# Optimization experiments

Hardware: AMD Instinct MI355X
Metric: run time of the kernel (lower is better)

The kernel has to match this reference:

```python
import jax, jax.numpy as jnp
import numpy as np
import math

NP, MNP, BS, DIM, NH, TOPK, FF = 512, 4096, 8, 256, 8, 32, 2048
HD = DIM // NH
EPS = 1e-5


def _ln(x, w, b):
    mu = jnp.mean(x, axis=-1, keepdims=True)
    var = jnp.mean((x - mu) ** 2, axis=-1, keepdims=True)
    return (x - mu) / jnp.sqrt(var + EPS) * w + b


def _lin(x, w, b):
    return x @ w.T + b


def setup_inputs() -> dict:
    key = jax.random.key(0)
    ks = jax.random.split(key, 16)
    s = 0.02
    d = {
        "tgt": jax.random.normal(ks[0], (NP, BS, DIM), jnp.float32),
        "memory": jax.random.normal(ks[1], (MNP, BS, DIM), jnp.float32),
        "query_pos": jax.random.normal(ks[2], (NP, BS, DIM), jnp.float32),
        "key_pos": jax.random.normal(ks[3], (MNP, BS, DIM), jnp.float32),
        "cw1": jax.random.normal(ks[4], (DIM, DIM), jnp.float32) * s,
        "cb1": jnp.zeros((DIM,), jnp.float32),
        "cw2": jax.random.normal(ks[5], (DIM, DIM), jnp.float32) * s,
        "cb2": jnp.zeros((DIM,), jnp.float32),
        "cw3": jax.random.normal(ks[6], (DIM, DIM), jnp.float32) * s,
        "cb3": jnp.zeros((DIM,), jnp.float32),
        "sa_in_w": jax.random.normal(ks[7], (3 * DIM, DIM), jnp.float32) * s,
        "sa_in_b": jnp.zeros((3 * DIM,), jnp.float32),
        "sa_out_w": jax.random.normal(ks[8], (DIM, DIM), jnp.float32) * s,
        "sa_out_b": jnp.zeros((DIM,), jnp.float32),
        "ln1_w": jnp.ones((DIM,), jnp.float32),
        "ln1_b": jnp.zeros((DIM,), jnp.float32),
        "ln2_w": jnp.ones((DIM,), jnp.float32),
        "ln2_b": jnp.zeros((DIM,), jnp.float32),
        "ln3_w": jnp.ones((DIM,), jnp.float32),
        "ln3_b": jnp.zeros((DIM,), jnp.float32),
        "ff1_w": jax.random.normal(ks[9], (FF, DIM), jnp.float32) * s,
        "ff1_b": jnp.zeros((FF,), jnp.float32),
        "ff2_w": jax.random.normal(ks[10], (DIM, FF), jnp.float32) * s,
        "ff2_b": jnp.zeros((DIM,), jnp.float32),
    }
    return d


def _forward(tgt, memory, query_pos, key_pos,
             cw1, cb1, cw2, cb2, cw3, cb3,
             sa_in_w, sa_in_b, sa_out_w, sa_out_b,
             ln1_w, ln1_b, ln2_w, ln2_b, ln3_w, ln3_b,
             ff1_w, ff1_b, ff2_w, ff2_b):
    npq, bs, dim = tgt.shape
    mnp = memory.shape[0]
    scale = 1.0 / math.sqrt(HD)

    # --- top-k cosine similarity neighbor selection (indices, non-diff) ---
    x = tgt.transpose(1, 0, 2)        # [bs, np, dim]
    m = memory.transpose(1, 0, 2)     # [bs, mnp, dim]
    xn = x / jnp.linalg.norm(x, axis=2, keepdims=True)
    mn = m / jnp.linalg.norm(m, axis=2, keepdims=True)
    sim = jnp.einsum('bnd,bmd->bnm', xn, mn)          # [bs, np, mnp]
    _, rns = jax.lax.top_k(sim, TOPK)                  # [bs, np, topk]

    # --- masked cross attention ---
    qc = (tgt + query_pos).transpose(1, 0, 2)          # [bs, np, dim]
    kc = (memory + key_pos).transpose(1, 0, 2)         # [bs, mnp, dim]
    vc = m
    qh = _lin(qc, cw1, cb1).reshape(bs, npq, NH, HD).transpose(0, 2, 1, 3)   # [bs,nh,np,hd]
    kh = _lin(kc, cw2, cb2).reshape(bs, mnp, NH, HD).transpose(0, 2, 1, 3)   # [bs,nh,mnp,hd]
    vh = _lin(vc, cw3, cb3).reshape(bs, mnp, NH, HD).transpose(0, 2, 1, 3)   # [bs,nh,mnp,hd]
    w = jnp.einsum('bhnd,bhmd->bhnm', qh, kh) * scale                         # [bs,nh,np,mnp]

    b_idx = jnp.arange(bs)[:, None, None]
    n_idx = jnp.arange(npq)[None, :, None]
    mask = jnp.zeros((bs, npq, mnp), w.dtype).at[b_idx, n_idx, rns].set(1.0)  # same for all heads
    mask = mask[:, None, :, :]                                                # [bs,1,np,mnp]
    w = w * mask + (-1e9) * (1.0 - mask)
    w = jax.nn.softmax(w, axis=3)
    cross = jnp.einsum('bhnm,bhmd->bhnd', w, vh).transpose(2, 0, 1, 3).reshape(npq, bs, dim)

    t = _ln(tgt + cross, ln1_w, ln1_b)

    # --- self attention (torch nn.MultiheadAttention, q=k=t+pos, v=t) ---
    wq, wk, wv = sa_in_w[:DIM], sa_in_w[DIM:2 * DIM], sa_in_w[2 * DIM:]
    bq, bk, bv = sa_in_b[:DIM], sa_in_b[DIM:2 * DIM], sa_in_b[2 * DIM:]
    qk = t + query_pos                                 # [np, bs, dim]
    q2 = _lin(qk, wq, bq).transpose(1, 0, 2).reshape(bs, npq, NH, HD).transpose(0, 2, 1, 3)
    k2 = _lin(qk, wk, bk).transpose(1, 0, 2).reshape(bs, npq, NH, HD).transpose(0, 2, 1, 3)
    v2 = _lin(t, wv, bv).transpose(1, 0, 2).reshape(bs, npq, NH, HD).transpose(0, 2, 1, 3)
    attn = jax.nn.softmax(jnp.einsum('bhnd,bhmd->bhnm', q2, k2) * scale, axis=-1)
    sa = jnp.einsum('bhnm,bhmd->bhnd', attn, v2).transpose(2, 0, 1, 3).reshape(npq, bs, dim)
    sa = _lin(sa, sa_out_w, sa_out_b)

    t = _ln(t + sa, ln2_w, ln2_b)

    # --- FFN (exact GELU, matching torch F.gelu default) ---
    ff = _lin(jax.nn.gelu(_lin(t, ff1_w, ff1_b), approximate=False), ff2_w, ff2_b)
    t = _ln(t + ff, ln3_w, ln3_b)
    return t


def reference(tgt, memory, query_pos, key_pos,
              cw1, cb1, cw2, cb2, cw3, cb3,
              sa_in_w, sa_in_b, sa_out_w, sa_out_b,
              ln1_w, ln1_b, ln2_w, ln2_b, ln3_w, ln3_b,
              ff1_w, ff1_b, ff2_w, ff2_b):
    return _forward(tgt, memory, query_pos, key_pos,
                    cw1, cb1, cw2, cb2, cw3, cb3,
                    sa_in_w, sa_in_b, sa_out_w, sa_out_b,
                    ln1_w, ln1_b, ln2_w, ln2_b, ln3_w, ln3_b,
                    ff1_w, ff1_b, ff2_w, ff2_b)
```

## Files before the change

kernel.cpp:

```cpp
#include <hip/hip_runtime.h>
#include <math.h>

typedef unsigned short u16;
typedef unsigned int u32;
typedef __bf16 bf16x8 __attribute__((ext_vector_type(8)));
typedef float f32x4 __attribute__((ext_vector_type(4)));

#define NPQ 512
#define MNP 4096
#define BSZ 8
#define DIM 256
#define NH 8
#define HD 32
#define TOPK 32
#define FFD 2048
#define SCALE 0.17677669529663687f

__device__ __forceinline__ u16 f2bf(float f){
  u32 u = __builtin_bit_cast(u32, f);
  u = (u + 0x7FFFu + ((u >> 16) & 1u)) >> 16;
  return (u16)u;
}
__device__ __forceinline__ float bf2f(u16 h){
  u32 u = ((u32)h) << 16;
  return __builtin_bit_cast(float, u);
}
__device__ __forceinline__ float wredsum(float v){
#pragma unroll
  for (int m = 32; m; m >>= 1) v += __shfl_xor(v, m, 64);
  return v;
}
__device__ __forceinline__ float gelu_exact(float x){
  return 0.5f * x * (1.0f + erff(x * 0.70710678118654752f));
}
__device__ __forceinline__ u32 keytr(u32 u){
  return u ^ (((u32)((int)u >> 31)) | 0x80000000u);
}

__global__ __launch_bounds__(256)
void cvt_all(const float* __restrict__ s0, const float* __restrict__ s1,
             const float* __restrict__ s2, const float* __restrict__ s3,
             const float* __restrict__ s4, const float* __restrict__ s5,
             const float* __restrict__ s6, u16* __restrict__ dst){
  int i = blockIdx.x*256 + threadIdx.x;
  if (i >= 1507328) return;
  const float* s; int base;
  if      (i <  65536){ s = s0; base = 0; }
  else if (i < 131072){ s = s1; base = 65536; }
  else if (i < 196608){ s = s2; base = 131072; }
  else if (i < 393216){ s = s3; base = 196608; }
  else if (i < 458752){ s = s4; base = 393216; }
  else if (i < 983040){ s = s5; base = 458752; }
  else                { s = s6; base = 983040; }
  dst[i] = f2bf(s[i - base]);
}

__global__ __launch_bounds__(256)
void prep_tgt(const float* __restrict__ tgt, const float* __restrict__ qpos,
              u16* __restrict__ xnh, u16* __restrict__ xnl, u16* __restrict__ qc,
              const float* __restrict__ cb2, const float* __restrict__ cb3,
              float* __restrict__ cbKV){
  __shared__ float sc[4];
  int r = blockIdx.x, t = threadIdx.x;
  if (r == 0){ cbKV[t] = cb2[t]; cbKV[256 + t] = cb3[t]; }
  int b = r >> 9, n = r & 511;
  long src = ((long)n*BSZ + b)*DIM + t;
  float x = tgt[src];
  float s = wredsum(x*x);
  if ((t & 63) == 0) sc[t >> 6] = s;
  __syncthreads();
  float tot = sc[0]+sc[1]+sc[2]+sc[3];
  float xn = x / sqrtf(tot);
  u16 hi = f2bf(xn);
  long dst = (long)r*DIM + t;
  xnh[dst] = hi;
  xnl[dst] = f2bf(xn - bf2f(hi));
  qc[dst]  = f2bf(x + qpos[src]);
}

__global__ __launch_bounds__(256)
void prep_mem(const float* __restrict__ mem, const float* __restrict__ kpos,
              u16* __restrict__ mnh, u16* __restrict__ mnl,
              u16* __restrict__ kc, u16* __restrict__ vc){
  __shared__ float sc[4];
  int r = blockIdx.x, t = threadIdx.x;
  int b = r >> 12, mp = r & 4095;
  long src = ((long)mp*BSZ + b)*DIM + t;
  float x = mem[src];
  float s = wredsum(x*x);
  if ((t & 63) == 0) sc[t >> 6] = s;
  __syncthreads();
  float tot = sc[0]+sc[1]+sc[2]+sc[3];
  float xn = x / sqrtf(tot);
  u16 hi = f2bf(xn);
  long dst = (long)r*DIM + t;
  mnh[dst] = hi;
  mnl[dst] = f2bf(xn - bf2f(hi));
  kc[dst]  = f2bf(x + kpos[src]);
  vc[dst]  = f2bf(x);
}

#define BST2 72
__global__ __launch_bounds__(256, 3)
void sim_gemm(const u16* __restrict__ xnh, const u16* __restrict__ xnl,
              const u16* __restrict__ mnh, const u16* __restrict__ mnl,
              float* __restrict__ sim){
  __shared__ __align__(16) u16 Bh[128*BST2];
  __shared__ __align__(16) u16 Bl[128*BST2];
  int t = threadIdx.x, lane = t & 63, wv = t >> 6;
  int ml = lane & 15, quad = lane >> 4;
  int b = blockIdx.z;
  int tM = blockIdx.y * 128 + (wv & 1) * 64;
  int tN = blockIdx.x * 128;
  int nloc = (wv >> 1) * 64;
  const u16* Ah = xnh + ((long)b*NPQ + tM + ml)*DIM;
  const u16* Al = xnl + ((long)b*NPQ + tM + ml)*DIM;
  f32x4 acc[4][4];
  f32x4 zer = {0.f,0.f,0.f,0.f};
#pragma unroll
  for (int i = 0; i < 4; i++)
#pragma unroll
    for (int j = 0; j < 4; j++) acc[i][j] = zer;

  int srow = t >> 3, scg = t & 7;
  for (int s = 0; s < 4; s++){
    int k0 = s * 64;
    if (s) __syncthreads();
#pragma unroll
    for (int p = 0; p < 4; p++){
      int r = p*32 + srow;
      long g = ((long)b*MNP + tN + r)*DIM + k0 + scg*8;
      *(uint4*)(&Bh[r*BST2 + scg*8]) = *(const uint4*)(mnh + g);
      *(uint4*)(&Bl[r*BST2 + scg*8]) = *(const uint4*)(mnl + g);
    }
    bf16x8 ca[4], ca2[4], na[4], na2[4];
#pragma unroll
    for (int i = 0; i < 4; i++){
      ca[i]  = *(const bf16x8*)(Ah + (long)i*16*DIM + k0 + quad*8);
      ca2[i] = *(const bf16x8*)(Al + (long)i*16*DIM + k0 + quad*8);
    }
    __syncthreads();
#pragma unroll
    for (int kkh = 0; kkh < 2; kkh++){
      int kk = kkh * 32;
      if (kkh == 0){
#pragma unroll
        for (int i = 0; i < 4; i++){
          na[i]  = *(const bf16x8*)(Ah + (long)i*16*DIM + k0 + 32 + quad*8);
          na2[i] = *(const bf16x8*)(Al + (long)i*16*DIM + k0 + 32 + quad*8);
        }
      }
      bf16x8 bh[4], bl[4];
#pragma unroll
      for (int j = 0; j < 4; j++){
        int nr = nloc + j*16 + ml;
        bh[j] = *(const bf16x8*)(&Bh[nr*BST2 + kk + quad*8]);
        bl[j] = *(const bf16x8*)(&Bl[nr*BST2 + kk + quad*8]);
      }
#pragma unroll
      for (int i = 0; i < 4; i++)
#pragma unroll
        for (int j = 0; j < 4; j++){
          acc[i][j] = __builtin_amdgcn_mfma_f32_16x16x32_bf16(ca[i],  bh[j], acc[i][j], 0, 0, 0);
          acc[i][j] = __builtin_amdgcn_mfma_f32_16x16x32_bf16(ca[i],  bl[j], acc[i][j], 0, 0, 0);
          acc[i][j] = __builtin_amdgcn_mfma_f32_16x16x32_bf16(ca2[i], bh[j], acc[i][j], 0, 0, 0);
        }
#pragma unroll
      for (int i = 0; i < 4; i++){ ca[i] = na[i]; ca2[i] = na2[i]; }
    }
  }
  long zC = (long)b * NPQ * MNP;
#pragma unroll
  for (int i = 0; i < 4; i++)
#pragma unroll
    for (int r = 0; r < 4; r++){
      int row = tM + i*16 + quad*4 + r;
#pragma unroll
      for (int j = 0; j < 4; j++){
        int col = tN + nloc + j*16 + ml;
        sim[zC + (long)row*MNP + col] = acc[i][j][r];
      }
    }
}

#define PBST 264
template<int KGROUPS, int OUT_BF16, int ACT>
__global__ __launch_bounds__(256)
void pgemm(const u16* __restrict__ A, const u16* __restrict__ A2, int selCol,
           const u16* __restrict__ B, const float* __restrict__ bias,
           void* __restrict__ Cv, int N){
  __shared__ __align__(16) u16 Bs[64*PBST];
  const int K = KGROUPS*256;
  int t = threadIdx.x, lane = t & 63, wv = t >> 6;
  int ml = lane & 15, quad = lane >> 4;
  int tM = blockIdx.x*64;
  int tN = blockIdx.y*64;
  const u16* Ab = (tN < selCol) ? A : A2;
  const u16* Arow = Ab + (long)(tM + wv*16 + ml)*K;
  f32x4 acc[4];
  f32x4 zer = {0.f,0.f,0.f,0.f};
#pragma unroll
  for (int nj = 0; nj < 4; nj++) acc[nj] = zer;
  int srow = t >> 5, scol = (t & 31)*8;
  for (int g = 0; g < KGROUPS; g++){
    if (g) __syncthreads();
#pragma unroll
    for (int p = 0; p < 8; p++){
      int r = p*8 + srow;
      *(uint4*)(&Bs[r*PBST + scol]) = *(const uint4*)(B + (long)(tN + r)*K + g*256 + scol);
    }
    bf16x8 a[8];
#pragma unroll
    for (int kk = 0; kk < 8; kk++)
      a[kk] = *(const bf16x8*)(Arow + g*256 + kk*32 + quad*8);
    __syncthreads();
#pragma unroll
    for (int kk = 0; kk < 8; kk++){
#pragma unroll
      for (int nj = 0; nj < 4; nj++){
        bf16x8 bv = *(const bf16x8*)(&Bs[(nj*16 + ml)*PBST + kk*32 + quad*8]);
        acc[nj] = __builtin_amdgcn_mfma_f32_16x16x32_bf16(a[kk], bv, acc[nj], 0, 0, 0);
      }
    }
  }
#pragma unroll
  for (int nj = 0; nj < 4; nj++){
    int col = tN + nj*16 + ml;
    float bv = bias[col];
#pragma unroll
    for (int r = 0; r < 4; r++){
      int row = tM + wv*16 + quad*4 + r;
      float v = acc[nj][r] + bv;
      if (ACT == 1) v = gelu_exact(v);
      long idx = (long)row * N + col;
      if (OUT_BF16) ((u16*)Cv)[idx] = f2bf(v);
      else ((float*)Cv)[idx] = v;
    }
  }
}

__global__ __launch_bounds__(256, 4)
void topk_k(const float* __restrict__ sim, int* __restrict__ rns){
  __shared__ int cnt_lds[2][2][32];
  __shared__ int cg_lds[2][2];
  __shared__ int scnt[2];
  __shared__ int stcnt[2];
  __shared__ int sties[2][64];
  int t = threadIdx.x, lane = t & 63, wv = t >> 6;
  int pair = wv >> 1, h = wv & 1;
  int r = blockIdx.x*2 + pair;
  const uint4* row4 = (const uint4*)(sim + (long)r * 4096);
  u32 key[32];
#pragma unroll
  for (int j = 0; j < 8; j++){
    uint4 v = row4[(h*8 + j)*64 + lane];
    key[j*4+0] = keytr(v.x);
    key[j*4+1] = keytr(v.y);
    key[j*4+2] = keytr(v.z);
    key[j*4+3] = keytr(v.w);
  }
#pragma unroll
  for (int i = 0; i < 32; i++) asm volatile("" : "+v"(key[i]));
  if (t < 2){ scnt[t] = 0; stcnt[t] = 0; }
  u32 pref = 0;
#pragma unroll 1
  for (int bit = 31; bit >= 0; bit--){
    u32 cand = pref | (1u << bit);
    int c = 0;
#pragma unroll
    for (int i = 0; i < 32; i++)
      c += (int)__popcll(__ballot(key[i] >= cand));
    if (lane == 0) cnt_lds[pair][h][bit] = c;
    __syncthreads();
    int cnt = cnt_lds[pair][0][bit] + cnt_lds[pair][1][bit];
    if (cnt >= TOPK) pref = cand;
  }
  int cg_w = 0;
#pragma unroll
  for (int i = 0; i < 32; i++)
    cg_w += (int)__popcll(__ballot(key[i] > pref));
  if (lane == 0) cg_lds[pair][h] = cg_w;
  __syncthreads();
  int cg = cg_lds[pair][0] + cg_lds[pair][1];
  int k_rem = TOPK - cg;
  int* out = rns + (long)r * 32;
#pragma unroll
  for (int i = 0; i < 32; i++){
    int gidx = (h*8 + (i >> 2))*256 + lane*4 + (i & 3);
    if (key[i] > pref){
      int p = atomicAdd(&scnt[pair], 1);
      out[p] = gidx;
    } else if (key[i] == pref){
      int p = atomicAdd(&stcnt[pair], 1);
      if (p < 64) sties[pair][p] = gidx;
    }
  }
  __syncthreads();
  if (h == 0 && lane == 0){
    int n = stcnt[pair]; if (n > 64) n = 64;
    for (int s = 0; s < k_rem; s++){
      int mb = 0;
      for (int j = 1; j < n; j++) if (sties[pair][j] < sties[pair][mb]) mb = j;
      out[cg + s] = sties[pair][mb];
      sties[pair][mb] = 0x7FFFFFFF;
    }
  }
}

#define CAS 272
__global__ __launch_bounds__(256)
void cross_attn(const u16* __restrict__ qh, const u16* __restrict__ khvh,
                const int* __restrict__ rns, float* __restrict__ crossO){
  __shared__ __align__(16) u16 Kg[32*CAS];
  __shared__ __align__(16) u16 Vg[32*CAS];
  __shared__ float qv[256];
  __shared__ int idxs[32];
  __shared__ float L[256];
  __shared__ float pm[8], ps[8];
  int r = blockIdx.x, t = threadIdx.x;
  int b = r >> 9;
  if (t < 32) idxs[t] = rns[(long)r*32 + t];
  qv[t] = bf2f(qh[(long)r*DIM + t]);
  __syncthreads();
  for (int i = t; i < 32*64; i += 256){
    int k = i >> 6, c = (i & 63) * 4;
    long src = ((long)b*MNP + idxs[k])*512 + c;
    *(ushort4*)(&Kg[k*CAS + c]) = *(const ushort4*)(khvh + src);
    *(ushort4*)(&Vg[k*CAS + c]) = *(const ushort4*)(khvh + src + 256);
  }
  __syncthreads();
  {
    int h = t >> 5, k = t & 31;
    float acc = 0.f;
#pragma unroll
    for (int d = 0; d < 32; d++) acc += qv[h*HD + d] * bf2f(Kg[k*CAS + h*HD + d]);
    L[t] = acc * SCALE;
  }
  __syncthreads();
  if (t < 8){
    float m = L[t*32];
    for (int k = 1; k < 32; k++) m = fmaxf(m, L[t*32 + k]);
    float s = 0.f;
    for (int k = 0; k < 32; k++) s += expf(L[t*32 + k] - m);
    pm[t] = m; ps[t] = s;
  }
  __syncthreads();
  {
    int h = t >> 5, dd = t & 31;
    float m = pm[h], inv = 1.0f/ps[h], acc = 0.f;
#pragma unroll
    for (int k = 0; k < 32; k++) acc += expf(L[h*32 + k] - m) * bf2f(Vg[k*CAS + h*HD + dd]);
    crossO[(long)r*DIM + t] = acc * inv;
  }
}

template<int MODE>
__global__ __launch_bounds__(256)
void ln_k(const float* __restrict__ xa, const float* __restrict__ xb,
          const float* __restrict__ qpos,
          const float* __restrict__ w, const float* __restrict__ bsh,
          float* __restrict__ yf, u16* __restrict__ yb, u16* __restrict__ qkb){
  __shared__ float sc[8];
  int r = blockIdx.x, t = threadIdx.x;
  int b = r >> 9, n = r & 511;
  long bidx = (long)r*DIM + t;
  long nidx = ((long)n*BSZ + b)*DIM + t;
  float x = (MODE == 1 ? xa[nidx] : xa[bidx]) + xb[bidx];
  float s  = wredsum(x);
  float s2 = wredsum(x*x);
  int wv = t >> 6;
  if ((t & 63) == 0){ sc[wv] = s; sc[4 + wv] = s2; }
  __syncthreads();
  float S  = sc[0]+sc[1]+sc[2]+sc[3];
  float S2 = sc[4]+sc[5]+sc[6]+sc[7];
  float mu  = S * (1.f/256.f);
  float var = S2 * (1.f/256.f) - mu*mu;
  float y = (x - mu) * (1.0f / sqrtf(var + 1e-5f)) * w[t] + bsh[t];
  if (MODE == 3){
    yf[nidx] = y;
  } else {
    yf[bidx] = y;
    yb[bidx] = f2bf(y);
    if (MODE == 1) qkb[bidx] = f2bf(y + qpos[nidx]);
  }
}

#define KST 40
#define PST 264
__global__ __launch_bounds__(256)
void self_attn(const u16* __restrict__ qkv, u16* __restrict__ sa_pre){
  __shared__ __align__(16) u16 KS[512*KST];
  __shared__ __align__(16) u16 QS[32*KST];
  __shared__ float mbuf[128];
  __shared__ float sbuf[128];
  u16* P  = KS;
  u16* Vt = KS + 32*PST;

  int qt = blockIdx.x, h = blockIdx.y, b = blockIdx.z;
  int t = threadIdx.x, lane = t & 63, wv = t >> 6;
  int ml = lane & 15, quad = lane >> 4;
  int n0 = qt * 32;

  {
    int q = t >> 3, d4 = (t & 7) * 4;
    const u16* src = qkv + ((long)b*NPQ + n0 + q)*768 + h*HD + d4;
    *(ushort2*)(QS + q*KST + d4)     = *(const ushort2*)(src);
    *(ushort2*)(QS + q*KST + d4 + 2) = *(const ushort2*)(src + 2);
  }
  for (int i = t; i < 512*8; i += 256){
    int j = i >> 3, d4 = (i & 7) * 4;
    const u16* src = qkv + ((long)b*NPQ + j)*768 + 256 + h*HD + d4;
    *(ushort2*)(KS + j*KST + d4)     = *(const ushort2*)(src);
    *(ushort2*)(KS + j*KST + d4 + 2) = *(const ushort2*)(src + 2);
  }
  __syncthreads();

  f32x4 acc[2][8];
  {
    bf16x8 aq[2];
#pragma unroll
    for (int mi = 0; mi < 2; mi++)
      aq[mi] = *(const bf16x8*)(QS + (mi*16 + ml)*KST + quad*8);
#pragma unroll
    for (int nj = 0; nj < 8; nj++){
      bf16x8 bk = *(const bf16x8*)(KS + (wv*128 + nj*16 + ml)*KST + quad*8);
      f32x4 z = {0.f,0.f,0.f,0.f};
#pragma unroll
      for (int mi = 0; mi < 2; mi++)
        acc[mi][nj] = __builtin_amdgcn_mfma_f32_16x16x32_bf16(aq[mi], bk, z, 0, 0, 0);
    }
  }
  float lmax[2][4];
#pragma unroll
  for (int mi = 0; mi < 2; mi++)
#pragma unroll
    for (int r = 0; r < 4; r++) lmax[mi][r] = -3.4e38f;
#pragma unroll
  for (int mi = 0; mi < 2; mi++)
#pragma unroll
    for (int nj = 0; nj < 8; nj++)
#pragma unroll
      for (int r = 0; r < 4; r++){
        float v = acc[mi][nj][r] * SCALE;
        acc[mi][nj][r] = v;
        lmax[mi][r] = fmaxf(lmax[mi][r], v);
      }
#pragma unroll
  for (int m = 1; m < 16; m <<= 1)
#pragma unroll
    for (int mi = 0; mi < 2; mi++)
#pragma unroll
      for (int r = 0; r < 4; r++)
        lmax[mi][r] = fmaxf(lmax[mi][r], __shfl_xor(lmax[mi][r], m, 64));
  if (ml == 0){
#pragma unroll
    for (int mi = 0; mi < 2; mi++)
#pragma unroll
      for (int r = 0; r < 4; r++)
        mbuf[(mi*16 + quad*4 + r)*4 + wv] = lmax[mi][r];
  }
  __syncthreads();
  float inv_[2][4];
  float lsum[2][4];
#pragma unroll
  for (int mi = 0; mi < 2; mi++)
#pragma unroll
    for (int r = 0; r < 4; r++){
      int row = mi*16 + quad*4 + r;
      float m0 = fmaxf(fmaxf(mbuf[row*4+0], mbuf[row*4+1]),
                       fmaxf(mbuf[row*4+2], mbuf[row*4+3]));
      float s = 0.f;
#pragma unroll
      for (int nj = 0; nj < 8; nj++){
        float e = __expf(acc[mi][nj][r] - m0);
        acc[mi][nj][r] = e;
        s += e;
      }
      lsum[mi][r] = s;
    }
#pragma unroll
  for (int m = 1; m < 16; m <<= 1)
#pragma unroll
    for (int mi = 0; mi < 2; mi++)
#pragma unroll
      for (int r = 0; r < 4; r++)
        lsum[mi][r] += __shfl_xor(lsum[mi][r], m, 64);
  if (ml == 0){
#pragma unroll
    for (int mi = 0; mi < 2; mi++)
#pragma unroll
      for (int r = 0; r < 4; r++)
        sbuf[(mi*16 + quad*4 + r)*4 + wv] = lsum[mi][r];
  }
  __syncthreads();
#pragma unroll
  for (int mi = 0; mi < 2; mi++)
#pragma unroll
    for (int r = 0; r < 4; r++){
      int row = mi*16 + quad*4 + r;
      inv_[mi][r] = 1.0f / (sbuf[row*4+0]+sbuf[row*4+1]+sbuf[row*4+2]+sbuf[row*4+3]);
    }

  int mi2 = wv >> 1, ni = wv & 1;
  f32x4 acc2 = {0.f,0.f,0.f,0.f};
  for (int half = 0; half < 2; half++){
    __syncthreads();
    if ((wv >> 1) == half){
      int cbase = (wv & 1) * 128;
#pragma unroll
      for (int mi = 0; mi < 2; mi++)
#pragma unroll
        for (int nj = 0; nj < 8; nj++)
#pragma unroll
          for (int r = 0; r < 4; r++)
            P[(mi*16 + quad*4 + r)*PST + cbase + nj*16 + ml] = f2bf(acc[mi][nj][r]);
    }
    for (int i = t; i < 2048; i += 256){
      int j = i >> 3, d4 = (i & 7) * 4;
      const u16* src = qkv + ((long)b*NPQ + half*256 + j)*768 + 512 + h*HD + d4;
      u16 v0 = src[0], v1 = src[1], v2e = src[2], v3 = src[3];
      Vt[(d4+0)*PST + j] = v0;
      Vt[(d4+1)*PST + j] = v1;
      Vt[(d4+2)*PST + j] = v2e;
      Vt[(d4+3)*PST + j] = v3;
    }
    __syncthreads();
#pragma unroll
    for (int k0 = 0; k0 < 256; k0 += 32){
      bf16x8 ap = *(const bf16x8*)(P  + (mi2*16 + ml)*PST + k0 + quad*8);
      bf16x8 bv = *(const bf16x8*)(Vt + (ni*16  + ml)*PST + k0 + quad*8);
      acc2 = __builtin_amdgcn_mfma_f32_16x16x32_bf16(ap, bv, acc2, 0, 0, 0);
    }
  }
#pragma unroll
  for (int r = 0; r < 4; r++){
    int row = mi2*16 + quad*4 + r;
    sa_pre[((long)b*NPQ + n0 + row)*DIM + h*HD + ni*16 + ml] =
        f2bf(acc2[r] * inv_[mi2][r]);
  }
}

extern "C" void kernel_launch(void* const* d_in, const int* in_sizes, int n_in,
                              void* d_out, int out_size, void* d_ws, size_t ws_size,
                              hipStream_t stream){
  (void)in_sizes; (void)n_in; (void)out_size; (void)ws_size;
  const float* tgt  = (const float*)d_in[0];
  const float* mem  = (const float*)d_in[1];
  const float* qpos = (const float*)d_in[2];
  const float* kpos = (const float*)d_in[3];
  const float* cw1  = (const float*)d_in[4];  const float* cb1 = (const float*)d_in[5];
  const float* cw2  = (const float*)d_in[6];  const float* cb2 = (const float*)d_in[7];
  const float* cw3  = (const float*)d_in[8];  const float* cb3 = (const float*)d_in[9];
  const float* saw  = (const float*)d_in[10]; const float* sab = (const float*)d_in[11];
  const float* sow  = (const float*)d_in[12]; const float* sob = (const float*)d_in[13];
  const float* ln1w = (const float*)d_in[14]; const float* ln1b = (const float*)d_in[15];
  const float* ln2w = (const float*)d_in[16]; const float* ln2b = (const float*)d_in[17];
  const float* ln3w = (const float*)d_in[18]; const float* ln3b = (const float*)d_in[19];
  const float* f1w  = (const float*)d_in[20]; const float* f1bs = (const float*)d_in[21];
  const float* f2w  = (const float*)d_in[22]; const float* f2bs = (const float*)d_in[23];

  char* base = (char*)d_ws;
  size_t off = 0;
  auto alloc = [&](size_t bytes) -> char* {
    char* p = base + off;
    off += (bytes + 255) & ~(size_t)255;
    return p;
  };
  u16* cw1b = (u16*)alloc(65536u*2);
  u16* cw2b = (u16*)alloc(65536u*2);
  u16* cw3b = (u16*)alloc(65536u*2);   (void)cw3b;
  u16* sawb = (u16*)alloc(196608u*2);
  u16* sowb = (u16*)alloc(65536u*2);
  u16* f1wb = (u16*)alloc(524288u*2);
  u16* f2wb = (u16*)alloc(524288u*2);
  int* rns  = (int*)alloc(4096u*32*4);
  float* cbKV = (float*)alloc(512*4);
  size_t offB = off;
  u16* xnh = (u16*)alloc((size_t)4096*256*2);
  u16* xnl = (u16*)alloc((size_t)4096*256*2);
  u16* mnh = (u16*)alloc((size_t)32768*256*2);
  u16* mnl = (u16*)alloc((size_t)32768*256*2);
  u16* qc  = (u16*)alloc((size_t)4096*256*2);
  u16* kc  = (u16*)alloc((size_t)32768*256*2);
  u16* vc  = (u16*)alloc((size_t)32768*256*2);
  float* sim = (float*)alloc((size_t)8*512*4096*4);

  char* regC = (char*)sim;
  u16* qh   = (u16*)regC;
  u16* khvh = (u16*)(regC + 2097152);
  char* regB = base + offB;
  size_t ob = 0;
  auto allocB = [&](size_t bytes) -> char* {
    char* p = regB + ob;
    ob += (bytes + 255) & ~(size_t)255;
    return p;
  };
  float* cross = (float*)allocB((size_t)4096*256*4);
  float* t1    = (float*)allocB((size_t)4096*256*4);
  u16*   t1b   = (u16*)allocB((size_t)4096*256*2);
  u16*   qkb   = (u16*)allocB((size_t)4096*256*2);
  u16*   qkv   = (u16*)allocB((size_t)4096*768*2);
  u16*   sa_pre= (u16*)allocB((size_t)4096*256*2);
  float* sa    = (float*)allocB((size_t)4096*256*4);
  float* t2    = (float*)allocB((size_t)4096*256*4);
  u16*   t2b   = (u16*)allocB((size_t)4096*256*2);
  u16*   h1    = (u16*)allocB((size_t)4096*2048*2);
  float* ff    = (float*)allocB((size_t)4096*256*4);

  const int BIG = 1 << 30;
  dim3 blk(256);
  cvt_all<<<dim3((1507328 + 255)/256), blk, 0, stream>>>(
      cw1, cw2, cw3, saw, sow, f1w, f2w, cw1b);
  prep_tgt<<<dim3(4096), blk, 0, stream>>>(tgt, qpos, xnh, xnl, qc, cb2, cb3, cbKV);
  prep_mem<<<dim3(32768), blk, 0, stream>>>(mem, kpos, mnh, mnl, kc, vc);
  sim_gemm<<<dim3(32,4,8), blk, 0, stream>>>(xnh, xnl, mnh, mnl, sim);
  topk_k<<<dim3(2048), blk, 0, stream>>>(sim, rns);
  pgemm<1,1,0><<<dim3(64,4), blk, 0, stream>>>(qc, qc, BIG, cw1b, cb1, qh, 256);
  pgemm<1,1,0><<<dim3(512,8), blk, 0, stream>>>(kc, vc, 256, cw2b, cbKV, khvh, 512);
  cross_attn<<<dim3(4096), blk, 0, stream>>>(qh, khvh, rns, cross);
  ln_k<1><<<dim3(4096), blk, 0, stream>>>(tgt, cross, qpos, ln1w, ln1b, t1, t1b, qkb);
  pgemm<1,1,0><<<dim3(64,12), blk, 0, stream>>>(qkb, t1b, 512, sawb, sab, qkv, 768);
  self_attn<<<dim3(16,8,8), blk, 0, stream>>>(qkv, sa_pre);
  pgemm<1,0,0><<<dim3(64,4), blk, 0, stream>>>(sa_pre, sa_pre, BIG, sowb, sob, sa, 256);
  ln_k<2><<<dim3(4096), blk, 0, stream>>>(t1, sa, nullptr, ln2w, ln2b, t2, t2b, nullptr);
  pgemm<1,1,1><<<dim3(64,32), blk, 0, stream>>>(t2b, t2b, BIG, f1wb, f1bs, h1, 2048);
  pgemm<8,0,0><<<dim3(64,4), blk, 0, stream>>>(h1, h1, BIG, f2wb, f2bs, ff, 256);
  ln_k<3><<<dim3(4096), blk, 0, stream>>>(t2, ff, nullptr, ln3w, ln3b, (float*)d_out, nullptr, nullptr);
}
```

Baseline: 429.7 us.

## Replace bitwise top-k radix select with 8-bit histogram radix select

The top-k selection kernel now runs one row per 256-thread block and finds the k-th key with four 8-bit histogram rounds using LDS atomics and a wave prefix scan. This replaces the previous 32 bit-by-bit ballot passes, each followed by a block barrier. Tie handling now allows up to 256 tied candidates, and the grid doubles to 4096 blocks. In exchange it adds shared-memory atomic contention on the histogram bins.

```diff
diff --git a/kernel.cpp b/kernel.cpp
--- a/kernel.cpp
+++ b/kernel.cpp
@@ -241,68 +241,82 @@
 
 __global__ __launch_bounds__(256, 4)
 void topk_k(const float* __restrict__ sim, int* __restrict__ rns){
-  __shared__ int cnt_lds[2][2][32];
-  __shared__ int cg_lds[2][2];
-  __shared__ int scnt[2];
-  __shared__ int stcnt[2];
-  __shared__ int sties[2][64];
-  int t = threadIdx.x, lane = t & 63, wv = t >> 6;
-  int pair = wv >> 1, h = wv & 1;
-  int r = blockIdx.x*2 + pair;
-  const uint4* row4 = (const uint4*)(sim + (long)r * 4096);
-  u32 key[32];
-#pragma unroll
-  for (int j = 0; j < 8; j++){
-    uint4 v = row4[(h*8 + j)*64 + lane];
+  __shared__ int hist[256];
+  __shared__ int sh_B, sh_above;
+  __shared__ int scnt, stcnt;
+  __shared__ int sties[256];
+  int t = threadIdx.x;
+  long r = blockIdx.x;
+  const uint4* row4 = (const uint4*)(sim + r*4096);
+  u32 key[16];
+#pragma unroll
+  for (int j = 0; j < 4; j++){
+    uint4 v = row4[j*256 + t];
     key[j*4+0] = keytr(v.x);
     key[j*4+1] = keytr(v.y);
     key[j*4+2] = keytr(v.z);
     key[j*4+3] = keytr(v.w);
   }
 #pragma unroll
-  for (int i = 0; i < 32; i++) asm volatile("" : "+v"(key[i]));
-  if (t < 2){ scnt[t] = 0; stcnt[t] = 0; }
+  for (int i = 0; i < 16; i++) asm volatile("" : "+v"(key[i]));
+  if (t == 0){ scnt = 0; stcnt = 0; }
   u32 pref = 0;
+  int k_above = 0;
 #pragma unroll 1
-  for (int bit = 31; bit >= 0; bit--){
-    u32 cand = pref | (1u << bit);
-    int c = 0;
-#pragma unroll
-    for (int i = 0; i < 32; i++)
-      c += (int)__popcll(__ballot(key[i] >= cand));
-    if (lane == 0) cnt_lds[pair][h][bit] = c;
+  for (int round = 0; round < 4; round++){
+    int shift = 24 - round*8;
+    u32 pmask = (round == 0) ? 0u : (0xFFFFFFFFu << (shift + 8));
+    hist[t] = 0;
     __syncthreads();
-    int cnt = cnt_lds[pair][0][bit] + cnt_lds[pair][1][bit];
-    if (cnt >= TOPK) pref = cand;
-  }
-  int cg_w = 0;
-#pragma unroll
-  for (int i = 0; i < 32; i++)
-    cg_w += (int)__popcll(__ballot(key[i] > pref));
-  if (lane == 0) cg_lds[pair][h] = cg_w;
-  __syncthreads();
-  int cg = cg_lds[pair][0] + cg_lds[pair][1];
-  int k_rem = TOPK - cg;
-  int* out = rns + (long)r * 32;
-#pragma unroll
-  for (int i = 0; i < 32; i++){
-    int gidx = (h*8 + (i >> 2))*256 + lane*4 + (i & 3);
-    if (key[i] > pref){
-      int p = atomicAdd(&scnt[pair], 1);
+#pragma unroll
+    for (int i = 0; i < 16; i++){
+      if (((key[i] ^ pref) & pmask) == 0)
+        atomicAdd(&hist[(key[i] >> shift) & 255], 1);
+    }
+    __syncthreads();
+    if (t < 64){
+      int h0 = hist[t*4+0], h1 = hist[t*4+1], h2 = hist[t*4+2], h3 = hist[t*4+3];
+      int local = h0 + h1 + h2 + h3;
+      int s = local;
+#pragma unroll
+      for (int off = 1; off < 64; off <<= 1){
+        int v = __shfl_down(s, off, 64);
+        s += (t + off < 64) ? v : 0;
+      }
+      int excl = s - local;
+      int a3 = excl, a2 = a3 + h3, a1 = a2 + h2, a0 = a1 + h1;
+      int ka = k_above;
+      if (ka + a3 < TOPK && ka + a3 + h3 >= TOPK){ sh_B = t*4+3; sh_above = ka + a3; }
+      if (ka + a2 < TOPK && ka + a2 + h2 >= TOPK){ sh_B = t*4+2; sh_above = ka + a2; }
+      if (ka + a1 < TOPK && ka + a1 + h1 >= TOPK){ sh_B = t*4+1; sh_above = ka + a1; }
+      if (ka + a0 < TOPK && ka + a0 + h0 >= TOPK){ sh_B = t*4+0; sh_above = ka + a0; }
+    }
+    __syncthreads();
+    pref |= ((u32)sh_B) << shift;
+    k_above = sh_above;
+  }
+  int* out = rns + r*32;
+#pragma unroll
+  for (int i = 0; i < 16; i++){
+    int gidx = (i >> 2)*1024 + t*4 + (i & 3);
+    u32 kk = key[i];
+    if (kk > pref){
+      int p = atomicAdd(&scnt, 1);
       out[p] = gidx;
-    } else if (key[i] == pref){
-      int p = atomicAdd(&stcnt[pair], 1);
-      if (p < 64) sties[pair][p] = gidx;
-    }
-  }
-  __syncthreads();
-  if (h == 0 && lane == 0){
-    int n = stcnt[pair]; if (n > 64) n = 64;
+    } else if (kk == pref){
+      int p = atomicAdd(&stcnt, 1);
+      if (p < 256) sties[p] = gidx;
+    }
+  }
+  __syncthreads();
+  if (t == 0){
+    int n = stcnt; if (n > 256) n = 256;
+    int k_rem = TOPK - k_above;
     for (int s = 0; s < k_rem; s++){
       int mb = 0;
-      for (int j = 1; j < n; j++) if (sties[pair][j] < sties[pair][mb]) mb = j;
-      out[cg + s] = sties[pair][mb];
-      sties[pair][mb] = 0x7FFFFFFF;
+      for (int j = 1; j < n; j++) if (sties[j] < sties[mb]) mb = j;
+      out[k_above + s] = sties[mb];
+      sties[mb] = 0x7FFFFFFF;
     }
   }
 }
@@ -614,7 +628,7 @@
   prep_tgt<<<dim3(4096), blk, 0, stream>>>(tgt, qpos, xnh, xnl, qc, cb2, cb3, cbKV);
   prep_mem<<<dim3(32768), blk, 0, stream>>>(mem, kpos, mnh, mnl, kc, vc);
   sim_gemm<<<dim3(32,4,8), blk, 0, stream>>>(xnh, xnl, mnh, mnl, sim);
-  topk_k<<<dim3(2048), blk, 0, stream>>>(sim, rns);
+  topk_k<<<dim3(4096), blk, 0, stream>>>(sim, rns);
   pgemm<1,1,0><<<dim3(64,4), blk, 0, stream>>>(qc, qc, BIG, cw1b, cb1, qh, 256);
   pgemm<1,1,0><<<dim3(512,8), blk, 0, stream>>>(kc, vc, 256, cw2b, cbKV, khvh, 512);
   cross_attn<<<dim3(4096), blk, 0, stream>>>(qh, khvh, rns, cross);
```

Result: no change. 425.9 us (-0.9%).
